# Optimization experiments

Hardware: AMD Instinct MI355X
Metric: run time of the kernel (lower is better)

The kernel has to match this reference:

```python
import jax, jax.numpy as jnp
import numpy as np

N = 100000   # nodes
F = 512      # in_channels
H = 128      # hidden_channels
HEADS = 2
E = 1600000  # edges
C = 64       # out_channels (classes)
EPS = 1e-5
GW = 0.8     # graph_weight


def setup_inputs() -> dict:
    key = jax.random.key(0)
    ks = jax.random.split(key, 16)
    rn = lambda k, s: jax.random.normal(k, s, jnp.float32) * 0.05
    return {
        'x': jax.random.normal(ks[0], (N, F), jnp.float32),
        'edge_index': jax.random.randint(ks[1], (2, E), 0, N),
        # TransConv params
        't_fc_w': rn(ks[2], (F, H)), 't_fc_b': jnp.zeros((H,), jnp.float32),
        't_ln0_g': jnp.ones((H,), jnp.float32), 't_ln0_b': jnp.zeros((H,), jnp.float32),
        't_wq_w': rn(ks[3], (H, H * HEADS)), 't_wq_b': jnp.zeros((H * HEADS,), jnp.float32),
        't_wk_w': rn(ks[4], (H, H * HEADS)), 't_wk_b': jnp.zeros((H * HEADS,), jnp.float32),
        't_wv_w': rn(ks[5], (H, H * HEADS)), 't_wv_b': jnp.zeros((H * HEADS,), jnp.float32),
        't_ln1_g': jnp.ones((H,), jnp.float32), 't_ln1_b': jnp.zeros((H,), jnp.float32),
        # GraphConv params
        'g_fc_w': rn(ks[6], (F, H)), 'g_fc_b': jnp.zeros((H,), jnp.float32),
        'g_bn0_g': jnp.ones((H,), jnp.float32), 'g_bn0_b': jnp.zeros((H,), jnp.float32),
        'g_conv_w': rn(ks[7], (H, H)), 'g_conv_b': jnp.zeros((H,), jnp.float32),
        'g_bn1_g': jnp.ones((H,), jnp.float32), 'g_bn1_b': jnp.zeros((H,), jnp.float32),
        # output fc
        'fc_w': rn(ks[8], (H, C)), 'fc_b': jnp.zeros((C,), jnp.float32),
    }


def _layernorm(x, g, b):
    mu = jnp.mean(x, axis=-1, keepdims=True)
    var = jnp.mean((x - mu) ** 2, axis=-1, keepdims=True)
    return (x - mu) * jax.lax.rsqrt(var + EPS) * g + b


def _batchnorm_eval(x, g, b):
    # eval-mode BN right after reset: running_mean=0, running_var=1
    return x * (1.0 / np.sqrt(1.0 + EPS)) * g + b


def _trans_conv(x, fc_w, fc_b, ln0_g, ln0_b, wq_w, wq_b, wk_w, wk_b, wv_w, wv_b, ln1_g, ln1_b):
    h = jax.nn.relu(_layernorm(x @ fc_w + fc_b, ln0_g, ln0_b))
    x0 = h
    n = h.shape[0]
    qs = (h @ wq_w + wq_b).reshape(n, HEADS, H)
    ks = (h @ wk_w + wk_b).reshape(n, HEADS, H)
    vs = (h @ wv_w + wv_b).reshape(n, HEADS, H)
    # global (Frobenius) norm, as in torch.norm(qs, p=2)
    qs = qs / jnp.linalg.norm(qs)
    ks = ks / jnp.linalg.norm(ks)
    kvs = jnp.einsum('lhm,lhd->hmd', ks, vs)                  # [h, m, d]
    attention_num = jnp.einsum('nhm,hmd->nhd', qs, kvs) + n * vs
    ks_sum = jnp.sum(ks, axis=0)                              # [h, m]
    normalizer = jnp.einsum('nhm,hm->nh', qs, ks_sum)[..., None] + float(n)
    attn_out = (attention_num / normalizer).mean(axis=1)       # [n, H]
    h = (attn_out + x0) / 2.0
    h = jax.nn.relu(_layernorm(h, ln1_g, ln1_b))
    return h


def _graph_conv(x, edge_index, fc_w, fc_b, bn0_g, bn0_b, conv_w, conv_b, bn1_g, bn1_b):
    h = jax.nn.relu(_batchnorm_eval(x @ fc_w + fc_b, bn0_g, bn0_b))
    x0 = h
    row, col = edge_index[0], edge_index[1]
    n = h.shape[0]
    deg = jax.ops.segment_sum(jnp.ones((row.shape[0],), jnp.float32), col, num_segments=n)
    val = jnp.sqrt(1.0 / deg[col]) * jnp.sqrt(1.0 / deg[row])
    val = jnp.nan_to_num(val, nan=0.0, posinf=0.0, neginf=0.0)
    agg = jax.ops.segment_sum(val[:, None] * h[row], col, num_segments=n)  # [n, H]
    h2 = agg @ conv_w + conv_b
    h2 = jax.nn.relu(_batchnorm_eval(h2, bn1_g, bn1_b))
    return h2 + x0


def reference(x, edge_index,
              t_fc_w, t_fc_b, t_ln0_g, t_ln0_b, t_wq_w, t_wq_b, t_wk_w, t_wk_b,
              t_wv_w, t_wv_b, t_ln1_g, t_ln1_b,
              g_fc_w, g_fc_b, g_bn0_g, g_bn0_b, g_conv_w, g_conv_b, g_bn1_g, g_bn1_b,
              fc_w, fc_b):
    x1 = _trans_conv(x, t_fc_w, t_fc_b, t_ln0_g, t_ln0_b, t_wq_w, t_wq_b,
                     t_wk_w, t_wk_b, t_wv_w, t_wv_b, t_ln1_g, t_ln1_b)
    x2 = _graph_conv(x, edge_index, g_fc_w, g_fc_b, g_bn0_g, g_bn0_b,
                     g_conv_w, g_conv_b, g_bn1_g, g_bn1_b)
    out = GW * x2 + (1.0 - GW) * x1
    return out @ fc_w + fc_b
```

## Files before the change

kernel.cpp:

```cpp
#include <hip/hip_runtime.h>

constexpr int N = 100000;
constexpr int F = 512;
constexpr int H = 128;
constexpr int E = 1600000;
constexpr int C = 64;
constexpr float EPS = 1e-5f;
constexpr float NF = 100000.0f;
constexpr float IBN = 0.999995000037f;

constexpr size_t OFF_HT   = 0;
constexpr size_t OFF_HG   = 12800000;
constexpr size_t OFF_AGG  = 25600000;
constexpr size_t OFF_CNT  = 38400000;
constexpr size_t OFF_S    = 38500000;
constexpr size_t OFF_G    = 38500128;
constexpr size_t OFF_PTR  = 38516512;
constexpr size_t OFF_CUR  = 38616512;
constexpr size_t OFF_BS   = 38716512;
constexpr size_t OFF_SROW = 38716640;
constexpr size_t OFF_SVAL = 40316640;
constexpr size_t OFF_GWV  = 41916640;
constexpr size_t OFF_KV   = OFF_GWV + 3 * 32768;
constexpr size_t OFF_KSUM = OFF_KV + 32768;
constexpr size_t OFF_VSUM = OFF_KSUM + 256;
constexpr size_t OFF_QSUM = OFF_VSUM + 256;
constexpr size_t OFF_SC   = OFF_QSUM + 256;
constexpr size_t OFF_B    = OFF_SC + 4;
constexpr size_t OFF_CC   = OFF_B + 32768;
constexpr size_t OFF_U    = OFF_CC + 256;
constexpr size_t OFF_U0   = OFF_U + 256;
constexpr size_t OFF_BT   = OFF_U0 + 4;

constexpr int NB1024 = (N + 1023) / 1024;
constexpr int NB_GRAM = (N + 255) / 256;
constexpr size_t SP_BASE = (size_t)NB_GRAM * 16384;

typedef __attribute__((ext_vector_type(8))) short short8;
typedef __attribute__((ext_vector_type(4))) float floatx4;

__device__ __forceinline__ float4 ld4(const float* p) {
  return *reinterpret_cast<const float4*>(p);
}
__device__ __forceinline__ void st4(float* p, float4 v) {
  *reinterpret_cast<float4*>(p) = v;
}
__device__ __forceinline__ unsigned short f2bf(float f) {
  unsigned u = __float_as_uint(f);
  u += 0x7fff + ((u >> 16) & 1);
  return (unsigned short)(u >> 16);
}
__device__ __forceinline__ float bf2f(unsigned short h) {
  return __uint_as_float((unsigned)h << 16);
}
__device__ __forceinline__ void gl_lds16(const unsigned short* g, unsigned short* l) {
  __builtin_amdgcn_global_load_lds(
      (const __attribute__((address_space(1))) unsigned int*)g,
      (__attribute__((address_space(3))) unsigned int*)l, 16, 0, 0);
}

__global__ __launch_bounds__(256) void k0_cvt(const float* __restrict__ Wt,
    const float* __restrict__ Wg, unsigned short* __restrict__ Bt)
{
  const int idx = blockIdx.x * 256 + threadIdx.x;
  const int k = idx >> 8;
  const int n = idx & 255;
  float v = (n < 128) ? Wt[(size_t)k * H + n] : Wg[(size_t)k * H + (n - 128)];
  const int kt = k >> 5;
  const int g  = (k >> 3) & 3;
  const int e  = k & 7;
  const int chunk = g * 256 + ((n + 2 * g) & 255);
  Bt[(((size_t)kt * 1024 + chunk) << 3) + e] = f2bf(v);
}

__global__ __launch_bounds__(512, 4) void k1_mfma(
    const float* __restrict__ x, const unsigned short* __restrict__ Bt,
    const float* __restrict__ bt, const float* __restrict__ lng, const float* __restrict__ lnb,
    const float* __restrict__ bgv, const float* __restrict__ bng, const float* __restrict__ bnb,
    float* __restrict__ ht, float* __restrict__ hg)
{
  __shared__ __align__(16) struct {
    unsigned short A[2][128 * 40];
    unsigned short B[2][8192];
  } sm;
  const int t = threadIdx.x;
  const int lane = t & 63;
  const int w = t >> 6;
  const int rq = (w >> 1) * 32;
  const int cq = (w & 1) * 128;
  const int g = lane >> 4;
  const int m = lane & 15;
  const int M0 = blockIdx.x * 128;

  floatx4 acc[2][8];
#pragma unroll
  for (int rt = 0; rt < 2; ++rt)
#pragma unroll
    for (int ct = 0; ct < 8; ++ct) acc[rt][ct] = (floatx4){0.f, 0.f, 0.f, 0.f};

  const int srow = t >> 2;
  const int scol8 = (t & 3) * 8;
  const int grow = (M0 + srow < N) ? (M0 + srow) : (N - 1);
  const float* xp = x + (size_t)grow * F + scol8;

  const int mb = cq + m + 2 * g;
  const int ldsw = (w << 6);

  {
#pragma unroll
    for (int i = 0; i < 2; ++i)
      gl_lds16(Bt + (((size_t)(i * 512 + t)) << 3),
               &sm.B[0][(size_t)(i * 512 + ldsw) << 3]);
    float4 a0 = ld4(xp), a1 = ld4(xp + 4);
    ushort4 p0, p1;
    p0.x = f2bf(a0.x); p0.y = f2bf(a0.y); p0.z = f2bf(a0.z); p0.w = f2bf(a0.w);
    p1.x = f2bf(a1.x); p1.y = f2bf(a1.y); p1.z = f2bf(a1.z); p1.w = f2bf(a1.w);
    *(ushort4*)(sm.A[0] + srow * 40 + scol8) = p0;
    *(ushort4*)(sm.A[0] + srow * 40 + scol8 + 4) = p1;
  }
  __syncthreads();

#pragma unroll 2
  for (int kt = 0; kt < 16; ++kt) {
    const int cur = kt & 1, nxt = cur ^ 1;
    float4 a0, a1;
    const bool more = (kt + 1 < 16);
    if (more) {
#pragma unroll
      for (int i = 0; i < 2; ++i)
        gl_lds16(Bt + (((size_t)(kt + 1) * 1024 + i * 512 + t) << 3),
                 &sm.B[nxt][(size_t)(i * 512 + ldsw) << 3]);
      a0 = ld4(xp + (kt + 1) * 32);
      a1 = ld4(xp + (kt + 1) * 32 + 4);
    }
    {
      const unsigned short* Ab = sm.A[cur];
      const unsigned short* Bb = sm.B[cur];
      short8 af[2], bf[8];
#pragma unroll
      for (int rt = 0; rt < 2; ++rt)
        af[rt] = *(const short8*)(Ab + (rq + rt * 16 + m) * 40 + g * 8);
#pragma unroll
      for (int ct = 0; ct < 8; ++ct) {
        const int chunk = g * 256 + ((mb + ct * 16) & 255);
        bf[ct] = *(const short8*)(Bb + ((size_t)chunk << 3));
      }
#pragma unroll
      for (int rt = 0; rt < 2; ++rt)
#pragma unroll
        for (int ct = 0; ct < 8; ++ct)
          acc[rt][ct] = __builtin_amdgcn_mfma_f32_16x16x32_bf16(af[rt], bf[ct], acc[rt][ct], 0, 0, 0);
    }
    if (more) {
      ushort4 p0, p1;
      p0.x = f2bf(a0.x); p0.y = f2bf(a0.y); p0.z = f2bf(a0.z); p0.w = f2bf(a0.w);
      p1.x = f2bf(a1.x); p1.y = f2bf(a1.y); p1.z = f2bf(a1.z); p1.w = f2bf(a1.w);
      *(ushort4*)(sm.A[nxt] + srow * 40 + scol8) = p0;
      *(ushort4*)(sm.A[nxt] + srow * 40 + scol8 + 4) = p1;
    }
    __syncthreads();
  }

  if (cq == 0) {
    float bt_l[8], lng_l[8], lnb_l[8];
#pragma unroll
    for (int ct = 0; ct < 8; ++ct) {
      bt_l[ct] = bt[ct * 16 + m];
      lng_l[ct] = lng[ct * 16 + m];
      lnb_l[ct] = lnb[ct * 16 + m];
    }
#pragma unroll
    for (int rt = 0; rt < 2; ++rt) {
#pragma unroll
      for (int r = 0; r < 4; ++r) {
        float sum = 0.f, sq = 0.f;
#pragma unroll
        for (int ct = 0; ct < 8; ++ct) {
          float v = acc[rt][ct][r] + bt_l[ct];
          acc[rt][ct][r] = v;
          sum += v; sq += v * v;
        }
#pragma unroll
        for (int off = 1; off < 16; off <<= 1) {
          sum += __shfl_xor(sum, off, 64);
          sq  += __shfl_xor(sq,  off, 64);
        }
        const float mu = sum * (1.f / H);
        const float rs = rsqrtf(sq * (1.f / H) - mu * mu + EPS);
        const int row = M0 + rq + rt * 16 + g * 4 + r;
        if (row < N) {
          float* hp = ht + (size_t)row * H + m;
#pragma unroll
          for (int ct = 0; ct < 8; ++ct) {
            float o = (acc[rt][ct][r] - mu) * rs * lng_l[ct] + lnb_l[ct];
            hp[ct * 16] = o > 0.f ? o : 0.f;
          }
        }
      }
    }
  } else {
#pragma unroll
    for (int ct = 0; ct < 8; ++ct) {
      const int c2 = ct * 16 + m;
      const float s1 = IBN * bng[c2], b0 = bgv[c2], b2v = bnb[c2];
#pragma unroll
      for (int rt = 0; rt < 2; ++rt) {
#pragma unroll
        for (int r = 0; r < 4; ++r) {
          const int row = M0 + rq + rt * 16 + g * 4 + r;
          if (row < N) {
            float v = (acc[rt][ct][r] + b0) * s1 + b2v;
            hg[(size_t)row * H + c2] = v > 0.f ? v : 0.f;
          }
        }
      }
    }
  }
}

__global__ __launch_bounds__(256) void k2_gram(const float* __restrict__ ht,
                                               float* __restrict__ gp,
                                               float* __restrict__ sp)
{
  const int t = threadIdx.x;
  const int b = blockIdx.x;
  const int base = b * 256;
  const int nend = (base + 256 < N) ? base + 256 : N;
  const int r0 = (t >> 4) * 8;
  const int c0 = (t & 15) * 8;
  float acc[8][8] = {};
  float colacc[8] = {};
  const bool do_col = (t < 16);
  int n = base;
  for (; n + 1 < nend; n += 2) {
    const float* hp0 = ht + (size_t)n * H;
    const float* hp1 = hp0 + H;
    float4 a00 = ld4(hp0 + r0), a01 = ld4(hp0 + r0 + 4);
    float4 b00 = ld4(hp0 + c0), b01 = ld4(hp0 + c0 + 4);
    float4 a10 = ld4(hp1 + r0), a11 = ld4(hp1 + r0 + 4);
    float4 b10 = ld4(hp1 + c0), b11 = ld4(hp1 + c0 + 4);
    float a0[8] = {a00.x, a00.y, a00.z, a00.w, a01.x, a01.y, a01.z, a01.w};
    float b0[8] = {b00.x, b00.y, b00.z, b00.w, b01.x, b01.y, b01.z, b01.w};
    float a1[8] = {a10.x, a10.y, a10.z, a10.w, a11.x, a11.y, a11.z, a11.w};
    float b1[8] = {b10.x, b10.y, b10.z, b10.w, b11.x, b11.y, b11.z, b11.w};
    if (do_col) {
#pragma unroll
      for (int j = 0; j < 8; ++j) colacc[j] += b0[j] + b1[j];
    }
#pragma unroll
    for (int i = 0; i < 8; ++i)
#pragma unroll
      for (int j = 0; j < 8; ++j)
        acc[i][j] += a0[i] * b0[j] + a1[i] * b1[j];
  }
  if (n < nend) {
    const float* hp0 = ht + (size_t)n * H;
    float4 a00 = ld4(hp0 + r0), a01 = ld4(hp0 + r0 + 4);
    float4 b00 = ld4(hp0 + c0), b01 = ld4(hp0 + c0 + 4);
    float a0[8] = {a00.x, a00.y, a00.z, a00.w, a01.x, a01.y, a01.z, a01.w};
    float b0[8] = {b00.x, b00.y, b00.z, b00.w, b01.x, b01.y, b01.z, b01.w};
    if (do_col) {
#pragma unroll
      for (int j = 0; j < 8; ++j) colacc[j] += b0[j];
    }
#pragma unroll
    for (int i = 0; i < 8; ++i)
#pragma unroll
      for (int j = 0; j < 8; ++j)
        acc[i][j] += a0[i] * b0[j];
  }
  float* g = gp + (size_t)b * 16384;
#pragma unroll
  for (int i = 0; i < 8; ++i) {
    st4(&g[(r0 + i) * H + c0], make_float4(acc[i][0], acc[i][1], acc[i][2], acc[i][3]));
    st4(&g[(r0 + i) * H + c0 + 4], make_float4(acc[i][4], acc[i][5], acc[i][6], acc[i][7]));
  }
  if (do_col) {
    float* spb = sp + (size_t)b * 128;
    st4(&spb[c0], make_float4(colacc[0], colacc[1], colacc[2], colacc[3]));
    st4(&spb[c0 + 4], make_float4(colacc[4], colacc[5], colacc[6], colacc[7]));
  }
}

__global__ __launch_bounds__(256) void k2r_reduce(const float* __restrict__ gp,
    const float* __restrict__ sp, float* __restrict__ G, float* __restrict__ s)
{
  const int i = blockIdx.x * 256 + threadIdx.x;
  float s0 = 0.f, s1 = 0.f, s2 = 0.f, s3 = 0.f;
  int b = 0;
  for (; b + 3 < NB_GRAM; b += 4) {
    s0 += gp[(size_t)b * 16384 + i];
    s1 += gp[(size_t)(b + 1) * 16384 + i];
    s2 += gp[(size_t)(b + 2) * 16384 + i];
    s3 += gp[(size_t)(b + 3) * 16384 + i];
  }
  for (; b < NB_GRAM; ++b) s0 += gp[(size_t)b * 16384 + i];
  G[i] = (s0 + s1) + (s2 + s3);
  if (blockIdx.x == 0 && threadIdx.x < 128) {
    float t0 = 0.f, t1 = 0.f;
    int bb = 0;
    for (; bb + 1 < NB_GRAM; bb += 2) {
      t0 += sp[(size_t)bb * 128 + threadIdx.x];
      t1 += sp[(size_t)(bb + 1) * 128 + threadIdx.x];
    }
    for (; bb < NB_GRAM; ++bb) t0 += sp[(size_t)bb * 128 + threadIdx.x];
    s[threadIdx.x] = t0 + t1;
  }
}

__global__ __launch_bounds__(256) void k3a_gw(const float* __restrict__ G,
    const float* __restrict__ Wv, const float* __restrict__ Wk,
    const float* __restrict__ Wq, float* __restrict__ GW)
{
  const int flat = blockIdx.x * 256 + threadIdx.x;
  const int w = flat >> 15;
  const int rem = flat & 32767;
  const int i = rem >> 8;
  const int j = rem & 255;
  const float* W = (w == 0) ? Wv : (w == 1) ? Wk : Wq;
  float sum = 0.f;
#pragma unroll 8
  for (int k = 0; k < H; ++k) sum += G[i * H + k] * W[k * 256 + j];
  GW[flat] = sum;
}

__global__ __launch_bounds__(256) void k3k_sums(const float* __restrict__ s,
    const float* __restrict__ Wk, const float* __restrict__ bk,
    const float* __restrict__ Wv, const float* __restrict__ bv,
    const float* __restrict__ Wq, const float* __restrict__ bq,
    float* __restrict__ ksum, float* __restrict__ vsum, float* __restrict__ qsum)
{
  const int flat = blockIdx.x * 256 + threadIdx.x;
  const int w = flat >> 8;
  const int j = flat & 255;
  const float* W = (w == 0) ? Wk : (w == 1) ? Wv : Wq;
  const float* b = (w == 0) ? bk : (w == 1) ? bv : bq;
  float* out = (w == 0) ? ksum : (w == 1) ? vsum : qsum;
  float sum = 0.f;
#pragma unroll 8
  for (int k = 0; k < H; ++k) sum += s[k] * W[k * 256 + j];
  out[j] = sum + NF * b[j];
}

__global__ __launch_bounds__(256) void k3b_kv(const float* __restrict__ GWv,
    const float* __restrict__ s, const float* __restrict__ Wk,
    const float* __restrict__ bk, const float* __restrict__ bv,
    const float* __restrict__ vsum, float* __restrict__ kv)
{
  const int flat = blockIdx.x * 256 + threadIdx.x;
  const int h = flat >> 14;
  const int m = (flat >> 7) & 127;
  const int d = flat & 127;
  float s1 = 0.f, s2 = 0.f;
#pragma unroll 4
  for (int k = 0; k < H; ++k) {
    float wkv = Wk[k * 256 + h * 128 + m];
    s1 += wkv * GWv[k * 256 + h * 128 + d];
    s2 += wkv * s[k];
  }
  kv[flat] = s1 + s2 * bv[h * 128 + d] + bk[h * 128 + m] * vsum[h * 128 + d];
}

__global__ __launch_bounds__(256) void k3c_ssq(
    const float* __restrict__ Wk, const float* __restrict__ GWk,
    const float* __restrict__ Wq, const float* __restrict__ GWq,
    const float* __restrict__ bk, const float* __restrict__ ksum,
    const float* __restrict__ bq, const float* __restrict__ qsum,
    float* __restrict__ sc)
{
  __shared__ float red[512];
  const int t = threadIdx.x;
  float pk = 0.f, pq = 0.f;
  for (int i = t; i < 32768; i += 256) {
    pk += Wk[i] * GWk[i];
    pq += Wq[i] * GWq[i];
  }
  pk += 2.f * bk[t] * ksum[t] - NF * bk[t] * bk[t];
  pq += 2.f * bq[t] * qsum[t] - NF * bq[t] * bq[t];
  red[t] = pk; red[256 + t] = pq;
  __syncthreads();
  for (int off = 128; off > 0; off >>= 1) {
    if (t < off) { red[t] += red[t + off]; red[256 + t] += red[256 + t + off]; }
    __syncthreads();
  }
  if (t == 0) {
    float ssq_k = red[0], ssq_q = red[256];
    sc[0] = ssq_q; sc[1] = ssq_k;
    sc[2] = rsqrtf(ssq_q * ssq_k);
  }
}

__global__ __launch_bounds__(256) void k3d_B(const float* __restrict__ Wq,
    const float* __restrict__ kv, const float* __restrict__ Wv,
    const float* __restrict__ sc, unsigned short* __restrict__ Bt2)
{
  const int flat = blockIdx.x * 256 + threadIdx.x;
  const int i = flat >> 8;
  const int j = flat & 255;
  const int h = j >> 7;
  const int d = j & 127;
  const float inv = sc[2];
  float sum = 0.f;
#pragma unroll 4
  for (int m = 0; m < H; ++m)
    sum += Wq[i * 256 + h * 128 + m] * kv[h * 16384 + m * 128 + d];
  Bt2[(size_t)j * H + i] = f2bf(sum * inv + NF * Wv[i * 256 + j]);
}

__global__ __launch_bounds__(512) void k3e_small(const float* __restrict__ bq,
    const float* __restrict__ kv, const float* __restrict__ bv,
    const float* __restrict__ Wq, const float* __restrict__ ksum,
    const float* __restrict__ sc, float* __restrict__ cc,
    float* __restrict__ u, float* __restrict__ u0)
{
  const int t = threadIdx.x;
  const float inv = sc[2];
  if (t < 256) {
    const int h = t >> 7, d = t & 127;
    float sum = 0.f;
    for (int m = 0; m < H; ++m) sum += bq[h * 128 + m] * kv[h * 16384 + m * 128 + d];
    cc[t] = sum * inv + NF * bv[t];
  } else {
    const int q = t - 256;
    const int i = q >> 1, h = q & 1;
    float sum = 0.f;
    for (int m = 0; m < H; ++m) sum += Wq[i * 256 + h * 128 + m] * ksum[h * 128 + m];
    u[i * 2 + h] = sum * inv;
  }
  if (t < 2) {
    float sum = 0.f;
    for (int m = 0; m < H; ++m) sum += bq[t * 128 + m] * ksum[t * 128 + m];
    u0[t] = sum * inv + NF;
  }
}

__global__ __launch_bounds__(256) void k4_mfma(float* __restrict__ ht,
    const unsigned short* __restrict__ Bt2, const float* __restrict__ cc,
    const float* __restrict__ u, const float* __restrict__ u0,
    const float* __restrict__ lng, const float* __restrict__ lnb)
{
  __shared__ __align__(16) union {
    unsigned short A[64 * 136];
    float lns[64 * 132];
  } sm;
  __shared__ float u_s[256];
  __shared__ float rden_s[128];
  __shared__ float mu_s[64], rs_s[64];
  const int t = threadIdx.x;
  const int lane = t & 63;
  const int w = t >> 6;
  const int rq = w * 16;
  const int g = lane >> 4;
  const int m = lane & 15;
  const int M0 = blockIdx.x * 64;

  {
    const int srow = t >> 2;
    const int scol = (t & 3) * 32;
    const int grow = (M0 + srow < N) ? (M0 + srow) : (N - 1);
    const float* xp = ht + (size_t)grow * H + scol;
#pragma unroll
    for (int j = 0; j < 8; ++j) {
      float4 a4 = ld4(xp + j * 4);
      ushort4 p;
      p.x = f2bf(a4.x); p.y = f2bf(a4.y); p.z = f2bf(a4.z); p.w = f2bf(a4.w);
      *(ushort4*)(sm.A + srow * 136 + scol + j * 4) = p;
    }
  }
  u_s[t] = u[t];
  __syncthreads();

  floatx4 acc[16];
#pragma unroll
  for (int ct = 0; ct < 16; ++ct) acc[ct] = (floatx4){0.f, 0.f, 0.f, 0.f};
#pragma unroll
  for (int kk = 0; kk < 128; kk += 32) {
    short8 af = *(const short8*)(sm.A + (rq + m) * 136 + kk + g * 8);
#pragma unroll
    for (int ct = 0; ct < 16; ++ct) {
      short8 bf = *(const short8*)(Bt2 + (size_t)(ct * 16 + m) * H + kk + g * 8);
      acc[ct] = __builtin_amdgcn_mfma_f32_16x16x32_bf16(af, bf, acc[ct], 0, 0, 0);
    }
  }
  if (t < 128) {
    const int row = t >> 1, head = t & 1;
    float den = u0[head];
    for (int k = 0; k < H; ++k)
      den += bf2f(sm.A[row * 136 + k]) * u_s[k * 2 + head];
    rden_s[row * 2 + head] = 0.5f / den;
  }
  __syncthreads();

#pragma unroll
  for (int ct = 0; ct < 8; ++ct) {
    const int d = ct * 16 + m;
    const float c0v = cc[d], c1v = cc[128 + d];
#pragma unroll
    for (int r = 0; r < 4; ++r) {
      const int row = rq + g * 4 + r;
      const int grow = M0 + row;
      const float rd0 = rden_s[row * 2], rd1 = rden_s[row * 2 + 1];
      float attn = (acc[ct][r] + c0v) * rd0 + (acc[ct + 8][r] + c1v) * rd1;
      float hres = (grow < N) ? ht[(size_t)grow * H + d] : 0.f;
      sm.lns[row * 132 + d] = (attn + hres) * 0.5f;
    }
  }
  __syncthreads();
  if (t < 64) {
    float sum = 0.f, sq = 0.f;
    for (int c2 = 0; c2 < H; ++c2) {
      float v = sm.lns[t * 132 + c2];
      sum += v; sq += v * v;
    }
    float mu = sum * (1.f / H);
    float var = sq * (1.f / H) - mu * mu;
    mu_s[t] = mu; rs_s[t] = rsqrtf(var + EPS);
  }
  __syncthreads();
  {
    const int r = t >> 2;
    const int cb = (t & 3) * 32;
    if (M0 + r < N) {
      const float mu = mu_s[r], rs = rs_s[r];
#pragma unroll
      for (int j = 0; j < 8; ++j) {
        const int c = cb + j * 4;
        float o[4];
#pragma unroll
        for (int q = 0; q < 4; ++q) {
          float v = (sm.lns[r * 132 + c + q] - mu) * rs * lng[c + q] + lnb[c + q];
          o[q] = v > 0.f ? v : 0.f;
        }
        st4(ht + (size_t)(M0 + r) * H + c, make_float4(o[0], o[1], o[2], o[3]));
      }
    }
  }
}

__global__ __launch_bounds__(256) void k5_deg(const int* __restrict__ ei,
                                              int* __restrict__ cnt)
{
  const int i = blockIdx.x * 256 + threadIdx.x;
  if (i < E) atomicAdd(&cnt[ei[E + i]], 1);
}

__global__ __launch_bounds__(256) void k_scan1(const int* __restrict__ cnt,
                                               int* __restrict__ bsum)
{
  __shared__ int red[256];
  const int t = threadIdx.x;
  const int base = blockIdx.x * 1024 + t * 4;
  int s = 0;
#pragma unroll
  for (int j = 0; j < 4; ++j) {
    int idx = base + j;
    if (idx < N) s += cnt[idx];
  }
  red[t] = s;
  __syncthreads();
  for (int off = 128; off > 0; off >>= 1) {
    if (t < off) red[t] += red[t + off];
    __syncthreads();
  }
  if (t == 0) bsum[blockIdx.x] = red[0];
}

__global__ __launch_bounds__(128) void k_scan2(int* __restrict__ bsum)
{
  __shared__ int sh[128];
  const int t = threadIdx.x;
  const int v = (t < NB1024) ? bsum[t] : 0;
  sh[t] = v;
  __syncthreads();
  for (int off = 1; off < 128; off <<= 1) {
    int add = (t >= off) ? sh[t - off] : 0;
    __syncthreads();
    sh[t] += add;
    __syncthreads();
  }
  if (t < NB1024) bsum[t] = sh[t] - v;
}

__global__ __launch_bounds__(256) void k_scan3(const int* __restrict__ cnt,
    const int* __restrict__ bsum, int* __restrict__ ptr, int* __restrict__ cur)
{
  __shared__ int part[256];
  const int t = threadIdx.x;
  const int base = blockIdx.x * 1024 + t * 4;
  int v[4];
  int tsum = 0;
#pragma unroll
  for (int j = 0; j < 4; ++j) {
    int idx = base + j;
    v[j] = (idx < N) ? cnt[idx] : 0;
    tsum += v[j];
  }
  part[t] = tsum;
  __syncthreads();
  for (int off = 1; off < 256; off <<= 1) {
    int add = (t >= off) ? part[t - off] : 0;
    __syncthreads();
    part[t] += add;
    __syncthreads();
  }
  int run = bsum[blockIdx.x] + part[t] - tsum;
#pragma unroll
  for (int j = 0; j < 4; ++j) {
    int idx = base + j;
    if (idx < N) { ptr[idx] = run; cur[idx] = run; }
    run += v[j];
  }
}

__global__ __launch_bounds__(256) void k6a_place(const int* __restrict__ ei,
    const int* __restrict__ cnt, int* __restrict__ cur,
    int* __restrict__ srow, float* __restrict__ sval)
{
  const int e = blockIdx.x * 256 + threadIdx.x;
  if (e >= E) return;
  const int r = ei[e];
  const int c = ei[E + e];
  const int p = atomicAdd(&cur[c], 1);
  srow[p] = r;
  const int dr = cnt[r];
  const float dv = (float)dr * (float)cnt[c];
  sval[p] = (dr > 0) ? rsqrtf(dv) : 0.f;
}

__global__ __launch_bounds__(256) void k6b_gather(const int* __restrict__ ptr,
    const int* __restrict__ cnt, const int* __restrict__ srow,
    const float* __restrict__ sval, const float* __restrict__ hg,
    float* __restrict__ agg)
{
  const int t = threadIdx.x;
  const int n = blockIdx.x * 8 + (t >> 5);
  const int lane4 = (t & 31) * 4;
  const int start = ptr[n];
  const int end = start + cnt[n];
  float4 acc = make_float4(0.f, 0.f, 0.f, 0.f);
  int e = start;
  for (; e + 3 < end; e += 4) {
    int r0 = srow[e], r1 = srow[e + 1], r2 = srow[e + 2], r3 = srow[e + 3];
    float v0 = sval[e], v1 = sval[e + 1], v2 = sval[e + 2], v3 = sval[e + 3];
    float4 h0 = ld4(hg + (size_t)r0 * H + lane4);
    float4 h1 = ld4(hg + (size_t)r1 * H + lane4);
    float4 h2 = ld4(hg + (size_t)r2 * H + lane4);
    float4 h3 = ld4(hg + (size_t)r3 * H + lane4);
    acc.x += v0 * h0.x + v1 * h1.x + v2 * h2.x + v3 * h3.x;
    acc.y += v0 * h0.y + v1 * h1.y + v2 * h2.y + v3 * h3.y;
    acc.z += v0 * h0.z + v1 * h1.z + v2 * h2.z + v3 * h3.z;
    acc.w += v0 * h0.w + v1 * h1.w + v2 * h2.w + v3 * h3.w;
  }
  for (; e < end; ++e) {
    int r0 = srow[e];
    float v0 = sval[e];
    float4 h0 = ld4(hg + (size_t)r0 * H + lane4);
    acc.x += v0 * h0.x;
    acc.y += v0 * h0.y;
    acc.z += v0 * h0.z;
    acc.w += v0 * h0.w;
  }
  st4(agg + (size_t)n * H + lane4, acc);
}

__global__ __launch_bounds__(256) void k78_out(const float* __restrict__ agg,
    const float* __restrict__ hg, const float* __restrict__ Wc,
    const float* __restrict__ cb, const float* __restrict__ g1,
    const float* __restrict__ b1, const float* __restrict__ ht,
    const float* __restrict__ fcW, const float* __restrict__ fcB,
    float* __restrict__ out)
{
  __shared__ float x2s[32][132];
  const int t = threadIdx.x;
  const int R0 = blockIdx.x * 32;
  {
    const int r0 = (t >> 5) * 4;
    const int c0 = (t & 31) * 4;
    float acc[4][4] = {};
    for (int k0 = 0; k0 < H; k0 += 4) {
      float ax[4][4];
#pragma unroll
      for (int r = 0; r < 4; ++r) {
        float4 a4 = ld4(agg + (size_t)(R0 + r0 + r) * H + k0);
        ax[r][0] = a4.x; ax[r][1] = a4.y; ax[r][2] = a4.z; ax[r][3] = a4.w;
      }
#pragma unroll
      for (int kk = 0; kk < 4; ++kk) {
        float4 w = ld4(Wc + (size_t)(k0 + kk) * H + c0);
#pragma unroll
        for (int r = 0; r < 4; ++r) {
          float av = ax[r][kk];
          acc[r][0] += av * w.x; acc[r][1] += av * w.y;
          acc[r][2] += av * w.z; acc[r][3] += av * w.w;
        }
      }
    }
#pragma unroll
    for (int r = 0; r < 4; ++r) {
      size_t off = (size_t)(R0 + r0 + r) * H + c0;
      float4 res = ld4(hg + off);
      float rsv[4] = {res.x, res.y, res.z, res.w};
#pragma unroll
      for (int j = 0; j < 4; ++j) {
        float v = (acc[r][j] + cb[c0 + j]) * IBN * g1[c0 + j] + b1[c0 + j];
        v = v > 0.f ? v : 0.f;
        x2s[r0 + r][c0 + j] = v + rsv[j];
      }
    }
  }
  __syncthreads();
  {
    const int rr0 = (t >> 4) * 2;
    const int c0 = (t & 15) * 4;
    float acc[2][4] = {};
    for (int k0 = 0; k0 < H; k0 += 4) {
      float ax[2][4];
#pragma unroll
      for (int r = 0; r < 2; ++r) {
        size_t off = (size_t)(R0 + rr0 + r) * H + k0;
        float4 a1 = ld4(ht + off);
        ax[r][0] = 0.2f * a1.x + 0.8f * x2s[rr0 + r][k0];
        ax[r][1] = 0.2f * a1.y + 0.8f * x2s[rr0 + r][k0 + 1];
        ax[r][2] = 0.2f * a1.z + 0.8f * x2s[rr0 + r][k0 + 2];
        ax[r][3] = 0.2f * a1.w + 0.8f * x2s[rr0 + r][k0 + 3];
      }
#pragma unroll
      for (int kk = 0; kk < 4; ++kk) {
        float4 w = ld4(fcW + (size_t)(k0 + kk) * C + c0);
#pragma unroll
        for (int r = 0; r < 2; ++r) {
          float av = ax[r][kk];
          acc[r][0] += av * w.x; acc[r][1] += av * w.y;
          acc[r][2] += av * w.z; acc[r][3] += av * w.w;
        }
      }
    }
#pragma unroll
    for (int r = 0; r < 2; ++r) {
      float o[4];
#pragma unroll
      for (int j = 0; j < 4; ++j) o[j] = acc[r][j] + fcB[c0 + j];
      st4(out + (size_t)(R0 + rr0 + r) * C + c0, make_float4(o[0], o[1], o[2], o[3]));
    }
  }
}

extern "C" void kernel_launch(void* const* d_in, const int* in_sizes, int n_in,
                              void* d_out, int out_size, void* d_ws, size_t ws_size,
                              hipStream_t stream) {
  (void)in_sizes; (void)n_in; (void)out_size; (void)ws_size;
  const float* x       = (const float*)d_in[0];
  const int*   ei      = (const int*)d_in[1];
  const float* t_fc_w  = (const float*)d_in[2];
  const float* t_fc_b  = (const float*)d_in[3];
  const float* t_ln0_g = (const float*)d_in[4];
  const float* t_ln0_b = (const float*)d_in[5];
  const float* t_wq_w  = (const float*)d_in[6];
  const float* t_wq_b  = (const float*)d_in[7];
  const float* t_wk_w  = (const float*)d_in[8];
  const float* t_wk_b  = (const float*)d_in[9];
  const float* t_wv_w  = (const float*)d_in[10];
  const float* t_wv_b  = (const float*)d_in[11];
  const float* t_ln1_g = (const float*)d_in[12];
  const float* t_ln1_b = (const float*)d_in[13];
  const float* g_fc_w  = (const float*)d_in[14];
  const float* g_fc_b  = (const float*)d_in[15];
  const float* g_bn0_g = (const float*)d_in[16];
  const float* g_bn0_b = (const float*)d_in[17];
  const float* g_cv_w  = (const float*)d_in[18];
  const float* g_cv_b  = (const float*)d_in[19];
  const float* g_bn1_g = (const float*)d_in[20];
  const float* g_bn1_b = (const float*)d_in[21];
  const float* fc_w    = (const float*)d_in[22];
  const float* fc_b    = (const float*)d_in[23];

  float* W    = (float*)d_ws;
  float* ht   = W + OFF_HT;
  float* hg   = W + OFF_HG;
  float* agg  = W + OFF_AGG;
  int*   cnt  = (int*)(W + OFF_CNT);
  float* s    = W + OFF_S;
  float* G    = W + OFF_G;
  int*   ptr  = (int*)(W + OFF_PTR);
  int*   cur  = (int*)(W + OFF_CUR);
  int*   bsum = (int*)(W + OFF_BS);
  int*   srow = (int*)(W + OFF_SROW);
  float* sval = W + OFF_SVAL;
  float* gw   = W + OFF_GWV;
  float* kv   = W + OFF_KV;
  float* ksum = W + OFF_KSUM;
  float* vsum = W + OFF_VSUM;
  float* qsum = W + OFF_QSUM;
  float* sc   = W + OFF_SC;
  unsigned short* Bt2 = (unsigned short*)(W + OFF_B);
  float* cc   = W + OFF_CC;
  float* u    = W + OFF_U;
  float* u0   = W + OFF_U0;
  unsigned short* Bt = (unsigned short*)(W + OFF_BT);

  hipMemsetAsync(cnt, 0, N * sizeof(int), stream);

  k0_cvt<<<512, 256, 0, stream>>>(t_fc_w, g_fc_w, Bt);

  k5_deg<<<(E + 255) / 256, 256, 0, stream>>>(ei, cnt);
  k_scan1<<<NB1024, 256, 0, stream>>>(cnt, bsum);
  k_scan2<<<1, 128, 0, stream>>>(bsum);
  k_scan3<<<NB1024, 256, 0, stream>>>(cnt, bsum, ptr, cur);
  k6a_place<<<E / 256, 256, 0, stream>>>(ei, cnt, cur, srow, sval);

  k1_mfma<<<(N + 127) / 128, 512, 0, stream>>>(x, Bt, t_fc_b, t_ln0_g, t_ln0_b,
                                               g_fc_b, g_bn0_g, g_bn0_b, ht, hg);
  k2_gram<<<NB_GRAM, 256, 0, stream>>>(ht, agg, agg + SP_BASE);
  k2r_reduce<<<64, 256, 0, stream>>>(agg, agg + SP_BASE, G, s);
  k6b_gather<<<N / 8, 256, 0, stream>>>(ptr, cnt, srow, sval, hg, agg);
  k3a_gw<<<384, 256, 0, stream>>>(G, t_wv_w, t_wk_w, t_wq_w, gw);
  k3k_sums<<<3, 256, 0, stream>>>(s, t_wk_w, t_wk_b, t_wv_w, t_wv_b, t_wq_w, t_wq_b,
                                  ksum, vsum, qsum);
  k3b_kv<<<128, 256, 0, stream>>>(gw, s, t_wk_w, t_wk_b, t_wv_b, vsum, kv);
  k3c_ssq<<<1, 256, 0, stream>>>(t_wk_w, gw + 32768, t_wq_w, gw + 65536,
                                 t_wk_b, ksum, t_wq_b, qsum, sc);
  k3d_B<<<128, 256, 0, stream>>>(t_wq_w, kv, t_wv_w, sc, Bt2);
  k3e_small<<<1, 512, 0, stream>>>(t_wq_b, kv, t_wv_b, t_wq_w, ksum, sc, cc, u, u0);
  k4_mfma<<<(N + 63) / 64, 256, 0, stream>>>(ht, Bt2, cc, u, u0, t_ln1_g, t_ln1_b);
  k78_out<<<N / 32, 256, 0, stream>>>(agg, hg, g_cv_w, g_cv_b, g_bn1_g, g_bn1_b,
                                      ht, fc_w, fc_b, (float*)d_out);
}
```

Measured before the change: 1.123 ms.

## Use bf16 MFMA for the graph-conv and output projections in the final kernel

Replaces the scalar FP32 FMA tiled GEMMs in the final output kernel with bf16 MFMA 16x16x32 instructions. A new conversion kernel transposes and packs the conv and output-fc weights to bf16. The aggregated features and the mixed hidden state are staged in LDS as bf16 between the two GEMMs. This removes the FP32 ALU bottleneck of the two small GEMMs over 100k rows, at the cost of reduced precision and an extra launch.

```diff
diff --git a/kernel.cpp b/kernel.cpp
--- a/kernel.cpp
+++ b/kernel.cpp
@@ -31,6 +31,8 @@
 constexpr size_t OFF_U    = OFF_CC + 256;
 constexpr size_t OFF_U0   = OFF_U + 256;
 constexpr size_t OFF_BT   = OFF_U0 + 4;
+constexpr size_t OFF_WCP  = OFF_BT + 65536;
+constexpr size_t OFF_FCP  = OFF_WCP + 8192;
 
 constexpr int NB1024 = (N + 1023) / 1024;
 constexpr int NB_GRAM = (N + 255) / 256;
@@ -71,6 +73,21 @@
   const int e  = k & 7;
   const int chunk = g * 256 + ((n + 2 * g) & 255);
   Bt[(((size_t)kt * 1024 + chunk) << 3) + e] = f2bf(v);
+}
+
+__global__ __launch_bounds__(256) void k0b_cvt(const float* __restrict__ Wc,
+    const float* __restrict__ fcW, unsigned short* __restrict__ Wcp,
+    unsigned short* __restrict__ fcp)
+{
+  const int idx = blockIdx.x * 256 + threadIdx.x;
+  if (idx < 16384) {
+    const int k = idx >> 7, n = idx & 127;
+    Wcp[(size_t)n * H + k] = f2bf(Wc[(size_t)k * H + n]);
+  } else {
+    const int q = idx - 16384;
+    const int k = q >> 6, n = q & 63;
+    fcp[(size_t)n * H + k] = f2bf(fcW[(size_t)k * C + n]);
+  }
 }
 
 __global__ __launch_bounds__(512, 4) void k1_mfma(
@@ -663,84 +680,91 @@
   st4(agg + (size_t)n * H + lane4, acc);
 }
 
-__global__ __launch_bounds__(256) void k78_out(const float* __restrict__ agg,
-    const float* __restrict__ hg, const float* __restrict__ Wc,
+__global__ __launch_bounds__(256) void k78_mfma(const float* __restrict__ agg,
+    const float* __restrict__ hg, const unsigned short* __restrict__ Wcp,
     const float* __restrict__ cb, const float* __restrict__ g1,
     const float* __restrict__ b1, const float* __restrict__ ht,
-    const float* __restrict__ fcW, const float* __restrict__ fcB,
+    const unsigned short* __restrict__ fcp, const float* __restrict__ fcB,
     float* __restrict__ out)
 {
-  __shared__ float x2s[32][132];
-  const int t = threadIdx.x;
-  const int R0 = blockIdx.x * 32;
+  __shared__ __align__(16) unsigned short A1[64 * 136];
+  const int t = threadIdx.x;
+  const int lane = t & 63;
+  const int w = t >> 6;
+  const int rq = w * 16;
+  const int g = lane >> 4;
+  const int m = lane & 15;
+  const int M0 = blockIdx.x * 64;
+
   {
-    const int r0 = (t >> 5) * 4;
-    const int c0 = (t & 31) * 4;
-    float acc[4][4] = {};
-    for (int k0 = 0; k0 < H; k0 += 4) {
-      float ax[4][4];
-#pragma unroll
-      for (int r = 0; r < 4; ++r) {
-        float4 a4 = ld4(agg + (size_t)(R0 + r0 + r) * H + k0);
-        ax[r][0] = a4.x; ax[r][1] = a4.y; ax[r][2] = a4.z; ax[r][3] = a4.w;
+    const int srow = t >> 2;
+    const int scol = (t & 3) * 32;
+    const int grow = (M0 + srow < N) ? (M0 + srow) : (N - 1);
+    const float* xp = agg + (size_t)grow * H + scol;
+#pragma unroll
+    for (int j = 0; j < 8; ++j) {
+      float4 a4 = ld4(xp + j * 4);
+      ushort4 p;
+      p.x = f2bf(a4.x); p.y = f2bf(a4.y); p.z = f2bf(a4.z); p.w = f2bf(a4.w);
+      *(ushort4*)(A1 + srow * 136 + scol + j * 4) = p;
+    }
+  }
+  __syncthreads();
+
+  floatx4 acc[8];
+#pragma unroll
+  for (int ct = 0; ct < 8; ++ct) acc[ct] = (floatx4){0.f, 0.f, 0.f, 0.f};
+#pragma unroll
+  for (int kk = 0; kk < 128; kk += 32) {
+    short8 af = *(const short8*)(A1 + (rq + m) * 136 + kk + g * 8);
+#pragma unroll
+    for (int ct = 0; ct < 8; ++ct) {
+      short8 bf = *(const short8*)(Wcp + (size_t)(ct * 16 + m) * H + kk + g * 8);
+      acc[ct] = __builtin_amdgcn_mfma_f32_16x16x32_bf16(af, bf, acc[ct], 0, 0, 0);
+    }
+  }
+  __syncthreads();
+
+#pragma unroll
+  for (int ct = 0; ct < 8; ++ct) {
+    const int col = ct * 16 + m;
+    const float s1 = IBN * g1[col], b0 = cb[col], b2v = b1[col];
+#pragma unroll
+    for (int r = 0; r < 4; ++r) {
+      const int row = rq + g * 4 + r;
+      const int grow = M0 + row;
+      float v = (acc[ct][r] + b0) * s1 + b2v;
+      v = v > 0.f ? v : 0.f;
+      float x1v = 0.f, hgv = 0.f;
+      if (grow < N) {
+        x1v = ht[(size_t)grow * H + col];
+        hgv = hg[(size_t)grow * H + col];
       }
-#pragma unroll
-      for (int kk = 0; kk < 4; ++kk) {
-        float4 w = ld4(Wc + (size_t)(k0 + kk) * H + c0);
-#pragma unroll
-        for (int r = 0; r < 4; ++r) {
-          float av = ax[r][kk];
-          acc[r][0] += av * w.x; acc[r][1] += av * w.y;
-          acc[r][2] += av * w.z; acc[r][3] += av * w.w;
-        }
-      }
-    }
+      A1[row * 136 + col] = f2bf(0.2f * x1v + 0.8f * (v + hgv));
+    }
+  }
+  __syncthreads();
+
+  floatx4 acc2[4];
+#pragma unroll
+  for (int ct = 0; ct < 4; ++ct) acc2[ct] = (floatx4){0.f, 0.f, 0.f, 0.f};
+#pragma unroll
+  for (int kk = 0; kk < 128; kk += 32) {
+    short8 af = *(const short8*)(A1 + (rq + m) * 136 + kk + g * 8);
+#pragma unroll
+    for (int ct = 0; ct < 4; ++ct) {
+      short8 bf = *(const short8*)(fcp + (size_t)(ct * 16 + m) * H + kk + g * 8);
+      acc2[ct] = __builtin_amdgcn_mfma_f32_16x16x32_bf16(af, bf, acc2[ct], 0, 0, 0);
+    }
+  }
+#pragma unroll
+  for (int ct = 0; ct < 4; ++ct) {
+    const int col = ct * 16 + m;
+    const float bb = fcB[col];
 #pragma unroll
     for (int r = 0; r < 4; ++r) {
-      size_t off = (size_t)(R0 + r0 + r) * H + c0;
-      float4 res = ld4(hg + off);
-      float rsv[4] = {res.x, res.y, res.z, res.w};
-#pragma unroll
-      for (int j = 0; j < 4; ++j) {
-        float v = (acc[r][j] + cb[c0 + j]) * IBN * g1[c0 + j] + b1[c0 + j];
-        v = v > 0.f ? v : 0.f;
-        x2s[r0 + r][c0 + j] = v + rsv[j];
-      }
-    }
-  }
-  __syncthreads();
-  {
-    const int rr0 = (t >> 4) * 2;
-    const int c0 = (t & 15) * 4;
-    float acc[2][4] = {};
-    for (int k0 = 0; k0 < H; k0 += 4) {
-      float ax[2][4];
-#pragma unroll
-      for (int r = 0; r < 2; ++r) {
-        size_t off = (size_t)(R0 + rr0 + r) * H + k0;
-        float4 a1 = ld4(ht + off);
-        ax[r][0] = 0.2f * a1.x + 0.8f * x2s[rr0 + r][k0];
-        ax[r][1] = 0.2f * a1.y + 0.8f * x2s[rr0 + r][k0 + 1];
-        ax[r][2] = 0.2f * a1.z + 0.8f * x2s[rr0 + r][k0 + 2];
-        ax[r][3] = 0.2f * a1.w + 0.8f * x2s[rr0 + r][k0 + 3];
-      }
-#pragma unroll
-      for (int kk = 0; kk < 4; ++kk) {
-        float4 w = ld4(fcW + (size_t)(k0 + kk) * C + c0);
-#pragma unroll
-        for (int r = 0; r < 2; ++r) {
-          float av = ax[r][kk];
-          acc[r][0] += av * w.x; acc[r][1] += av * w.y;
-          acc[r][2] += av * w.z; acc[r][3] += av * w.w;
-        }
-      }
-    }
-#pragma unroll
-    for (int r = 0; r < 2; ++r) {
-      float o[4];
-#pragma unroll
-      for (int j = 0; j < 4; ++j) o[j] = acc[r][j] + fcB[c0 + j];
-      st4(out + (size_t)(R0 + rr0 + r) * C + c0, make_float4(o[0], o[1], o[2], o[3]));
+      const int grow = M0 + rq + g * 4 + r;
+      if (grow < N) out[(size_t)grow * C + col] = acc2[ct][r] + bb;
     }
   }
 }
@@ -796,11 +820,14 @@
   float* cc   = W + OFF_CC;
   float* u    = W + OFF_U;
   float* u0   = W + OFF_U0;
-  unsigned short* Bt = (unsigned short*)(W + OFF_BT);
+  unsigned short* Bt  = (unsigned short*)(W + OFF_BT);
+  unsigned short* Wcp = (unsigned short*)(W + OFF_WCP);
+  unsigned short* fcp = (unsigned short*)(W + OFF_FCP);
 
   hipMemsetAsync(cnt, 0, N * sizeof(int), stream);
 
   k0_cvt<<<512, 256, 0, stream>>>(t_fc_w, g_fc_w, Bt);
+  k0b_cvt<<<96, 256, 0, stream>>>(g_cv_w, fc_w, Wcp, fcp);
 
   k5_deg<<<(E + 255) / 256, 256, 0, stream>>>(ei, cnt);
   k_scan1<<<NB1024, 256, 0, stream>>>(cnt, bsum);
@@ -822,6 +849,6 @@
   k3d_B<<<128, 256, 0, stream>>>(t_wq_w, kv, t_wv_w, sc, Bt2);
   k3e_small<<<1, 512, 0, stream>>>(t_wq_b, kv, t_wv_b, t_wq_w, ksum, sc, cc, u, u0);
   k4_mfma<<<(N + 63) / 64, 256, 0, stream>>>(ht, Bt2, cc, u, u0, t_ln1_g, t_ln1_b);
-  k78_out<<<N / 32, 256, 0, stream>>>(agg, hg, g_cv_w, g_cv_b, g_bn1_g, g_bn1_b,
-                                      ht, fc_w, fc_b, (float*)d_out);
-}
+  k78_mfma<<<(N + 63) / 64, 256, 0, stream>>>(agg, hg, Wcp, g_cv_b, g_bn1_g, g_bn1_b,
+                                              ht, fcp, fc_b, (float*)d_out);
+}
```

Result: faster. 1.020 ms (-9.2%).
